# Performance work log

Measured on AMD Instinct MI355X. Metric: run time of the kernel, lower is better.

## Reference

```python
import jax, jax.numpy as jnp
import numpy as np

N_PAIRS = 1_600_000   # total neighbor pairs (len(idx_i))
N_ATOMS = 50_000      # number of distinct center atoms (avg 32 neighbors each)


def setup_inputs() -> dict:
    key = jax.random.key(0)
    # sorted center indices -> consecutive ragged segments, like a neighbor list
    idx_i = jnp.sort(jax.random.randint(key, (N_PAIRS,), 0, N_ATOMS, dtype=jnp.int32))
    return {"idx_i": idx_i}


def reference(idx_i):
    # NOTE: output shape is data-dependent (sum_i C(c_i,2)), so this runs eagerly
    # (the concrete sizes below are python ints pulled from the input values),
    # exactly mirroring torch.unique_consecutive + per-segment torch.combinations.
    n = idx_i.shape[0]
    # --- unique_consecutive(return_counts=True), vectorized ---
    change = jnp.concatenate([jnp.ones((1,), bool), idx_i[1:] != idx_i[:-1]])
    seg_id = jnp.cumsum(change.astype(jnp.int32)) - 1          # [n] segment id per pair
    n_seg = int(seg_id[-1]) + 1
    counts = jnp.bincount(seg_id, length=n_seg)                 # [n_seg] c_i
    seg_off = jnp.concatenate([jnp.zeros((1,), counts.dtype), jnp.cumsum(counts)[:-1]])
    # --- per-segment number of unordered pairs C(c,2) ---
    tri_counts = counts * (counts - 1) // 2
    tri_off = jnp.concatenate([jnp.zeros((1,), tri_counts.dtype), jnp.cumsum(tri_counts)[:-1]])
    T = int(jnp.sum(tri_counts))
    # --- one flat vectorized pass over all T triples ---
    idx_i_triples = jnp.repeat(jnp.arange(n_seg, dtype=jnp.int32), tri_counts,
                               total_repeat_length=T)           # [T] segment index
    r = jnp.arange(T, dtype=counts.dtype) - tri_off[idx_i_triples]  # local triple rank
    c = counts[idx_i_triples]                                   # segment size per triple
    M = c * (c - 1) // 2
    rr = M - 1 - r                                              # rank counted from the end
    # triangular-root decode of condensed upper-triangle index (c is small -> fp32 exact)
    a_rev = jnp.floor((jnp.sqrt(8.0 * rr.astype(jnp.float32) + 1.0) - 1.0) / 2.0).astype(c.dtype)
    a = c - 2 - a_rev                                           # first local neighbor pos
    b = c - 1 - (rr - a_rev * (a_rev + 1) // 2)                 # second local neighbor pos (> a)
    base = seg_off[idx_i_triples]
    idx_j_triples = base + a
    idx_k_triples = base + b
    return (idx_i_triples, idx_j_triples, idx_k_triples)
```

## Files before the change

kernel.cpp:

```cpp
#include <hip/hip_runtime.h>

#define THREADS 256
#define EPT 8
#define FILL_BLOCKS 4096

__device__ __forceinline__ int blockReduceSum(int v, int* sdata) {
    int tid = threadIdx.x;
    sdata[tid] = v;
    __syncthreads();
    for (int off = THREADS >> 1; off > 0; off >>= 1) {
        if (tid < off) sdata[tid] += sdata[tid + off];
        __syncthreads();
    }
    int r = sdata[0];
    __syncthreads();
    return r;
}

__device__ __forceinline__ int blockScanIncl(int v, int* sdata) {
    int tid = threadIdx.x;
    sdata[tid] = v;
    __syncthreads();
    for (int off = 1; off < THREADS; off <<= 1) {
        int t = 0;
        if (tid >= off) t = sdata[tid - off];
        __syncthreads();
        if (tid >= off) sdata[tid] += t;
        __syncthreads();
    }
    int r = sdata[tid];
    __syncthreads();
    return r;
}

__device__ __forceinline__ int blockExclScanMax(int v, int* sdata) {
    int tid = threadIdx.x;
    sdata[tid] = v;
    __syncthreads();
    for (int off = 1; off < THREADS; off <<= 1) {
        int t = -1;
        if (tid >= off) t = sdata[tid - off];
        __syncthreads();
        if (tid >= off) sdata[tid] = max(sdata[tid], t);
        __syncthreads();
    }
    int r = (tid == 0) ? -1 : sdata[tid - 1];
    __syncthreads();
    return r;
}

__device__ int findPrevStart(const int* __restrict__ idx, int B0,
                             int* sdata, int* s_found) {
    int tid = threadIdx.x;
    if (tid == 0) *s_found = -1;
    __syncthreads();
    int res = -1;
    for (int step = 0; res < 0; ++step) {
        int p = B0 - 1 - step * THREADS - tid;
        int cand = -1;
        if (p >= 0) {
            bool f = (p == 0) || (idx[p - 1] != idx[p]);
            if (f) cand = p;
        }
        sdata[tid] = cand;
        __syncthreads();
        for (int off = THREADS >> 1; off > 0; off >>= 1) {
            if (tid < off) sdata[tid] = max(sdata[tid], sdata[tid + off]);
            __syncthreads();
        }
        if (tid == 0 && sdata[0] >= 0) *s_found = sdata[0];
        __syncthreads();
        res = *s_found;
        __syncthreads();
    }
    return res;
}

__global__ void k_chunkstats(const int* __restrict__ idx, int n,
                             int* __restrict__ chunkCnt,
                             int* __restrict__ chunkTriSum) {
    __shared__ int sdata[THREADS];
    __shared__ int s_tmp;
    int tid = threadIdx.x, bid = blockIdx.x;
    int B0 = bid * (THREADS * EPT);

    int prevStart = 0;
    if (bid > 0) prevStart = findPrevStart(idx, B0, sdata, &s_tmp);

    int base = B0 + tid * EPT;
    int cnt = 0, myLast = -1;
    for (int j = 0; j < EPT; ++j) {
        int p = base + j;
        if (p < n) {
            bool f = (p == 0) || (idx[p - 1] != idx[p]);
            if (f) { ++cnt; myLast = p; }
        }
    }
    int before = blockExclScanMax(myLast, sdata);
    int lastStart = max(prevStart, before);
    int sumq = 0;
    for (int j = 0; j < EPT; ++j) {
        int p = base + j;
        if (p < n) {
            if ((p == 0) || (idx[p - 1] != idx[p])) lastStart = p;
            sumq += p - lastStart;
        }
    }
    int c = blockReduceSum(cnt, sdata);
    int q = blockReduceSum(sumq, sdata);
    if (tid == 0) { chunkCnt[bid] = c; chunkTriSum[bid] = q; }
}

__global__ void k_emit(const int* __restrict__ idx, int n, int NB,
                       const int* __restrict__ chunkCnt,
                       const int* __restrict__ chunkTriSum,
                       int* __restrict__ segOff, int* __restrict__ triOff,
                       int* __restrict__ nsegPtr) {
    __shared__ int sdata[THREADS];
    __shared__ int s_tmp;
    int tid = threadIdx.x, bid = blockIdx.x;
    int B0 = bid * (THREADS * EPT);

    int prevStart = 0;
    if (bid > 0) prevStart = findPrevStart(idx, B0, sdata, &s_tmp);

    int pv = 0, tv = 0;
    for (int i = tid; i < bid; i += THREADS) {
        pv += chunkCnt[i];
        tv += chunkTriSum[i];
    }
    int segBase = blockReduceSum(pv, sdata);
    int triBase = blockReduceSum(tv, sdata);

    int base = B0 + tid * EPT;
    int cnt = 0, myLast = -1;
    for (int j = 0; j < EPT; ++j) {
        int p = base + j;
        if (p < n) {
            bool f = (p == 0) || (idx[p - 1] != idx[p]);
            if (f) { ++cnt; myLast = p; }
        }
    }
    int before = blockExclScanMax(myLast, sdata);
    int lastStart0 = max(prevStart, before);

    int lastStart = lastStart0;
    int sumq = 0;
    for (int j = 0; j < EPT; ++j) {
        int p = base + j;
        if (p < n) {
            if ((p == 0) || (idx[p - 1] != idx[p])) lastStart = p;
            sumq += p - lastStart;
        }
    }

    int inclC = blockScanIncl(cnt, sdata);
    int inclQ = blockScanIncl(sumq, sdata);
    int ord  = segBase + inclC - cnt;
    int tcur = triBase + inclQ - sumq;

    lastStart = lastStart0;
    for (int j = 0; j < EPT; ++j) {
        int p = base + j;
        if (p < n) {
            bool f = (p == 0) || (idx[p - 1] != idx[p]);
            if (f) {
                segOff[ord] = p;
                triOff[ord] = tcur;
                ++ord;
                lastStart = p;
            }
            tcur += p - lastStart;
        }
    }
    if (bid == NB - 1 && tid == THREADS - 1) {
        int nseg = segBase + inclC;
        *nsegPtr = nseg;
        segOff[nseg] = n;
    }
}

__global__ void k_fill(const int* __restrict__ segOff,
                       const int* __restrict__ triOff,
                       const int* __restrict__ nsegPtr,
                       int* __restrict__ outI, int* __restrict__ outJ,
                       int* __restrict__ outK) {
    int nseg = *nsegPtr;
    int wid = blockIdx.x * (THREADS / 64) + (threadIdx.x >> 6);
    int lane = threadIdx.x & 63;
    int nW = gridDim.x * (THREADS / 64);
    for (int s = wid; s < nseg; s += nW) {
        int baseP = segOff[s];
        int c = segOff[s + 1] - baseP;
        int M = c * (c - 1) / 2;
        int t0 = triOff[s];
        for (int r = lane; r < M; r += 64) {
            int rr = M - 1 - r;
            int k = (int)floorf((sqrtf((float)(8 * rr + 1)) - 1.0f) * 0.5f);
            if (k < 0) k = 0;
            while ((k + 1) * (k + 2) / 2 <= rr) ++k;
            while (k * (k + 1) / 2 > rr) --k;
            int a = c - 2 - k;
            int b = c - 1 - (rr - k * (k + 1) / 2);
            int t = t0 + r;
            outI[t] = s;
            outJ[t] = baseP + a;
            outK[t] = baseP + b;
        }
    }
}

extern "C" void kernel_launch(void* const* d_in, const int* in_sizes, int n_in,
                              void* d_out, int out_size, void* d_ws, size_t ws_size,
                              hipStream_t stream) {
    const int* idx = (const int*)d_in[0];
    int n = in_sizes[0];
    int T = out_size / 3;
    int* out = (int*)d_out;
    int* ws = (int*)d_ws;

    int* nsegPtr     = ws;
    int* chunkCnt    = ws + 16;
    int* chunkTriSum = ws + 16 + 8192;
    int* segOff      = ws + 16 + 16384;
    int* triOff      = segOff + (n + 1);

    int chunk = THREADS * EPT;
    int NB = (n + chunk - 1) / chunk;

    hipLaunchKernelGGL(k_chunkstats, dim3(NB), dim3(THREADS), 0, stream,
                       idx, n, chunkCnt, chunkTriSum);
    hipLaunchKernelGGL(k_emit, dim3(NB), dim3(THREADS), 0, stream,
                       idx, n, NB, chunkCnt, chunkTriSum,
                       segOff, triOff, nsegPtr);
    hipLaunchKernelGGL(k_fill, dim3(FILL_BLOCKS), dim3(THREADS), 0, stream,
                       segOff, triOff, nsegPtr, out, out + T, out + 2 * T);
}
```

Before: 83.46 us.

## Balance fill kernel by splitting output triples evenly across wavefronts

The fill kernel used to give each wavefront whole segments in round-robin order, so work per wave tracked segment sizes (quadratic in count) and many lanes sat idle on small segments. Each wavefront now owns an equal contiguous range of output triples, finds its starting segment by binary search over triOff, and walks segments clipping to its range. This evens out load and makes the stores contiguous per wave, at the cost of a binary search per wave and partial-segment bookkeeping.

```diff
diff --git a/kernel.cpp b/kernel.cpp
--- a/kernel.cpp
+++ b/kernel.cpp
@@ -182,19 +182,33 @@
 
 __global__ void k_fill(const int* __restrict__ segOff,
                        const int* __restrict__ triOff,
-                       const int* __restrict__ nsegPtr,
+                       const int* __restrict__ nsegPtr, int T,
                        int* __restrict__ outI, int* __restrict__ outJ,
                        int* __restrict__ outK) {
     int nseg = *nsegPtr;
-    int wid = blockIdx.x * (THREADS / 64) + (threadIdx.x >> 6);
+    int w = blockIdx.x * (THREADS / 64) + (threadIdx.x >> 6);
     int lane = threadIdx.x & 63;
     int nW = gridDim.x * (THREADS / 64);
-    for (int s = wid; s < nseg; s += nW) {
+    long long tlo = (long long)T * w / nW;
+    long long thi = (long long)T * (w + 1) / nW;
+    if (tlo >= thi) return;
+
+    int lo = 0, hi = nseg - 1;
+    while (lo < hi) {
+        int mid = (lo + hi + 1) >> 1;
+        if (triOff[mid] <= (int)tlo) lo = mid; else hi = mid - 1;
+    }
+    int s = lo;
+    long long t = tlo;
+    while (t < thi && s < nseg) {
         int baseP = segOff[s];
         int c = segOff[s + 1] - baseP;
         int M = c * (c - 1) / 2;
         int t0 = triOff[s];
-        for (int r = lane; r < M; r += 64) {
+        int rstart = (int)(t - t0);
+        int rend = M;
+        { long long cap = thi - t0; if (cap < (long long)rend) rend = (int)cap; }
+        for (int r = rstart + lane; r < rend; r += 64) {
             int rr = M - 1 - r;
             int k = (int)floorf((sqrtf((float)(8 * rr + 1)) - 1.0f) * 0.5f);
             if (k < 0) k = 0;
@@ -202,11 +216,13 @@
             while (k * (k + 1) / 2 > rr) --k;
             int a = c - 2 - k;
             int b = c - 1 - (rr - k * (k + 1) / 2);
-            int t = t0 + r;
-            outI[t] = s;
-            outJ[t] = baseP + a;
-            outK[t] = baseP + b;
-        }
+            int tt = t0 + r;
+            outI[tt] = s;
+            outJ[tt] = baseP + a;
+            outK[tt] = baseP + b;
+        }
+        t = (long long)t0 + rend;
+        ++s;
     }
 }
 
@@ -234,5 +250,5 @@
                        idx, n, NB, chunkCnt, chunkTriSum,
                        segOff, triOff, nsegPtr);
     hipLaunchKernelGGL(k_fill, dim3(FILL_BLOCKS), dim3(THREADS), 0, stream,
-                       segOff, triOff, nsegPtr, out, out + T, out + 2 * T);
-}
+                       segOff, triOff, nsegPtr, T, out, out + T, out + 2 * T);
+}
```

New measurement: 82.77 us. No clear change (-0.8%).
